# Optimization experiments

Measured on AMD Instinct MI355X. Metric: run time of the kernel, lower is better.

The kernel has to match this reference:

```python
import jax, jax.numpy as jnp
import numpy as np


def setup_inputs() -> dict:
    key = jax.random.key(0)
    kx, ky = jax.random.split(key)
    B, N, M = 32, 2048, 2048
    x = jax.random.normal(kx, (B, N, 3), dtype=jnp.float32)
    y = jax.random.normal(ky, (B, M, 3), dtype=jnp.float32)
    return {"x": x, "y": y}


def reference(x, y):
    # Faithful Chamfer distance matching the torch module.
    # Note: the original removes rows that sum exactly to 0; with random
    # float inputs no such rows exist, so that step is a no-op here.
    # d[b, i, j] = ||x[b, j] - y[b, i]||^2, shape [B, M, N]
    d = jnp.sum((x[:, None, :, :] - y[:, :, None, :]) ** 2, axis=-1)
    # min over y for each x point (dim 0 in the per-item [M, N] matrix)
    x_min = jnp.min(d, axis=1)  # [B, N]
    # min over x for each y point (dim 1)
    y_min = jnp.min(d, axis=2)  # [B, M]
    per_item = jnp.mean(x_min, axis=1) + jnp.mean(y_min, axis=1)  # [B]
    return jnp.mean(per_item)
```

## Files before the change

### kernel.cpp

```cpp
#include <hip/hip_runtime.h>


#define B_  32
#define N_  2048
#define PTS (B_ * N_)
#define ONEB 0x3F80u

typedef short  bf16x8 __attribute__((ext_vector_type(8)));
typedef float  f32x16 __attribute__((ext_vector_type(16)));

__device__ __forceinline__ unsigned short f2b(float f) {
    unsigned u = __float_as_uint(f);
    return (unsigned short)((u + 0x7FFFu + ((u >> 16) & 1u)) >> 16);
}
__device__ __forceinline__ float b2f(unsigned short h) {
    return __uint_as_float(((unsigned)h) << 16);
}
#define PK(a, b) (((unsigned)(a)) | (((unsigned)(b)) << 16))

__device__ __forceinline__ float min16(const f32x16 d) {
    const float a = fminf(fminf(d[0],  d[1]),  d[2]);
    const float b = fminf(fminf(d[3],  d[4]),  d[5]);
    const float c = fminf(fminf(d[6],  d[7]),  d[8]);
    const float e = fminf(fminf(d[9],  d[10]), d[11]);
    const float f = fminf(fminf(d[12], d[13]), d[14]);
    const float g = fminf(fminf(a, b), c);
    const float i = fminf(fminf(e, f), d[15]);
    return fminf(g, i);
}

__global__ __launch_bounds__(512, 4) void chamfer_mfma_kernel(
    const float* __restrict__ x, const float* __restrict__ y,
    float* __restrict__ partial)
{
    __shared__ unsigned sB[N_ * 8];
    __shared__ float pm[2][4][64];
    __shared__ float sred[4];

    const int bid  = blockIdx.x;
    const int dir  = bid >> 8;
    const int b    = (bid >> 3) & 31;
    const int qg   = bid & 7;
    const int tid  = threadIdx.x;
    const int lane = tid & 63;
    const int wv   = tid >> 6;
    const int qs2  = wv & 3;
    const int half = wv >> 2;
    const int h    = lane >> 5;
    const int ln31 = lane & 31;

    const float* q = dir ? y : x;
    const float* r = dir ? x : y;
    const float* rb = r + (size_t)b * N_ * 3;
    const float* qb = q + ((size_t)b * N_ + qg * 256 + qs2 * 64) * 3;

    for (int p = tid; p < N_; p += 512) {
        const float vx = rb[3 * p + 0], vy = rb[3 * p + 1], vz = rb[3 * p + 2];
        const unsigned short xh = f2b(vx), xl = f2b(vx - b2f(xh));
        const unsigned short yh = f2b(vy), yl = f2b(vy - b2f(yh));
        const unsigned short zh = f2b(vz), zl = f2b(vz - b2f(zh));
        const float nrm = fmaf(vx, vx, fmaf(vy, vy, vz * vz));
        const unsigned short nh = f2b(nrm), nl = f2b(nrm - b2f(nh));
        const unsigned base = ((unsigned)(p >> 5)) * 256u + ((unsigned)(p & 31)) * 4u;
        const uint4 lo = make_uint4(PK(xh, xl), PK(xh, xl), PK(yh, yl), PK(yh, yl));
        const uint4 hi = make_uint4(PK(zh, zl), PK(zh, zl), PK(nh, nl), PK(ONEB, ONEB));
        *(uint4*)(sB + base)        = lo;
        *(uint4*)(sB + base + 128)  = hi;
    }

    bf16x8 bq[2];
    #pragma unroll
    for (int s = 0; s < 2; ++s) {
        const float* qp = qb + (size_t)(s * 32 + ln31) * 3;
        const float vx = qp[0], vy = qp[1], vz = qp[2];
        const unsigned short xh = f2b(vx), xl = f2b(vx - b2f(xh));
        const unsigned short yh = f2b(vy), yl = f2b(vy - b2f(yh));
        const unsigned short zh = f2b(vz), zl = f2b(vz - b2f(zh));
        const float nrm = fmaf(vx, vx, fmaf(vy, vy, vz * vz));
        const unsigned short nh = f2b(nrm), nl = f2b(nrm - b2f(nh));
        const unsigned short mxh = f2b(-2.0f * b2f(xh)), mxl = f2b(-2.0f * b2f(xl));
        const unsigned short myh = f2b(-2.0f * b2f(yh)), myl = f2b(-2.0f * b2f(yl));
        const unsigned short mzh = f2b(-2.0f * b2f(zh)), mzl = f2b(-2.0f * b2f(zl));
        unsigned u[4];
        if (h == 0) {
            u[0] = PK(mxh, mxh); u[1] = PK(mxl, mxl);
            u[2] = PK(myh, myh); u[3] = PK(myl, myl);
        } else {
            u[0] = PK(mzh, mzh); u[1] = PK(mzl, mzl);
            u[2] = PK(ONEB, ONEB); u[3] = PK(nh, nl);
        }
        bq[s] = *(bf16x8*)u;
    }
    __syncthreads();

    const f32x16 zacc = {};
    float mac00 = 3.4e38f, mac01 = 3.4e38f;
    float mac10 = 3.4e38f, mac11 = 3.4e38f;
    const unsigned roff = (unsigned)h * 128u + (unsigned)ln31 * 4u;
    const unsigned* sBh = sB + half * 32 * 256;

    #pragma unroll 2
    for (int t = 0; t < 32; ++t) {
        const bf16x8 af = *(const bf16x8*)(sBh + t * 256 + roff);
        const f32x16 d0 = __builtin_amdgcn_mfma_f32_32x32x16_bf16(af, bq[0], zacc, 0, 0, 0);
        const f32x16 d1 = __builtin_amdgcn_mfma_f32_32x32x16_bf16(af, bq[1], zacc, 0, 0, 0);
        if (t & 1) { mac01 = fminf(mac01, min16(d0)); mac11 = fminf(mac11, min16(d1)); }
        else       { mac00 = fminf(mac00, min16(d0)); mac10 = fminf(mac10, min16(d1)); }
    }

    float m0 = fminf(mac00, mac01);
    float m1 = fminf(mac10, mac11);
    m0 = fminf(m0, __shfl_xor(m0, 32));
    m1 = fminf(m1, __shfl_xor(m1, 32));
    if (lane < 32) {
        pm[half][qs2][ln31]      = m0;
        pm[half][qs2][32 + ln31] = m1;
    }
    __syncthreads();

    if (tid < 256) {
        const float v = fminf(pm[0][tid >> 6][tid & 63],
                              pm[1][tid >> 6][tid & 63]);
        float s = v;
        s += __shfl_xor(s, 1);
        s += __shfl_xor(s, 2);
        s += __shfl_xor(s, 4);
        s += __shfl_xor(s, 8);
        s += __shfl_xor(s, 16);
        s += __shfl_xor(s, 32);
        if (lane == 0) sred[tid >> 6] = s;
    }
    __syncthreads();
    if (tid == 0) partial[bid] = (sred[0] + sred[1]) + (sred[2] + sred[3]);
}

__global__ __launch_bounds__(256) void chamfer_final_kernel(
    const float* __restrict__ partial, float* __restrict__ out)
{
    const int tid = threadIdx.x;
    float s = partial[tid] + partial[tid + 256];
    #pragma unroll
    for (int off = 32; off > 0; off >>= 1) s += __shfl_down(s, off);
    __shared__ float sr[4];
    if ((tid & 63) == 0) sr[tid >> 6] = s;
    __syncthreads();
    if (tid == 0)
        out[0] = ((sr[0] + sr[1]) + (sr[2] + sr[3])) * (1.0f / (float)PTS);
}

extern "C" void kernel_launch(void* const* d_in, const int* in_sizes, int n_in,
                              void* d_out, int out_size, void* d_ws, size_t ws_size,
                              hipStream_t stream)
{
    const float* x = (const float*)d_in[0];
    const float* y = (const float*)d_in[1];
    float* partial = (float*)d_ws;
    float* out     = (float*)d_out;

    chamfer_mfma_kernel<<<512, 512, 0, stream>>>(x, y, partial);
    chamfer_final_kernel<<<1, 256, 0, stream>>>(partial, out);
}
```

Baseline: 16.94 us.

## Fuse final reduction via atomicAdd, vectorize reference loads, fully unroll MFMA loop

Removes the second reduction kernel by having each block atomically add its scaled partial sum into the output, which is zeroed with a memset beforehand. The reference-point staging loop now loads four points per thread with three float4 reads instead of scalar strided loads. The MFMA inner loop is fully unrolled and the row offset is folded into the base pointer. The atomic accumulation makes the summation order nondeterministic, adds a memset launch, and the full unroll raises register pressure.

```diff
diff --git a/kernel.cpp b/kernel.cpp
--- a/kernel.cpp
+++ b/kernel.cpp
@@ -31,7 +31,7 @@
 
 __global__ __launch_bounds__(512, 4) void chamfer_mfma_kernel(
     const float* __restrict__ x, const float* __restrict__ y,
-    float* __restrict__ partial)
+    float* __restrict__ out)
 {
     __shared__ unsigned sB[N_ * 8];
     __shared__ float pm[2][4][64];
@@ -54,18 +54,28 @@
     const float* rb = r + (size_t)b * N_ * 3;
     const float* qb = q + ((size_t)b * N_ + qg * 256 + qs2 * 64) * 3;
 
-    for (int p = tid; p < N_; p += 512) {
-        const float vx = rb[3 * p + 0], vy = rb[3 * p + 1], vz = rb[3 * p + 2];
-        const unsigned short xh = f2b(vx), xl = f2b(vx - b2f(xh));
-        const unsigned short yh = f2b(vy), yl = f2b(vy - b2f(yh));
-        const unsigned short zh = f2b(vz), zl = f2b(vz - b2f(zh));
-        const float nrm = fmaf(vx, vx, fmaf(vy, vy, vz * vz));
-        const unsigned short nh = f2b(nrm), nl = f2b(nrm - b2f(nh));
-        const unsigned base = ((unsigned)(p >> 5)) * 256u + ((unsigned)(p & 31)) * 4u;
-        const uint4 lo = make_uint4(PK(xh, xl), PK(xh, xl), PK(yh, yl), PK(yh, yl));
-        const uint4 hi = make_uint4(PK(zh, zl), PK(zh, zl), PK(nh, nl), PK(ONEB, ONEB));
-        *(uint4*)(sB + base)        = lo;
-        *(uint4*)(sB + base + 128)  = hi;
+    {
+        const int p0 = tid * 4;
+        const float4* src = (const float4*)(rb + 3 * p0);
+        const float4 v0 = src[0], v1 = src[1], v2 = src[2];
+        const float px[4] = {v0.x, v0.w, v1.z, v2.y};
+        const float py[4] = {v0.y, v1.x, v1.w, v2.z};
+        const float pz[4] = {v0.z, v1.y, v2.x, v2.w};
+        #pragma unroll
+        for (int k = 0; k < 4; ++k) {
+            const int p = p0 + k;
+            const float vx = px[k], vy = py[k], vz = pz[k];
+            const unsigned short xh = f2b(vx), xl = f2b(vx - b2f(xh));
+            const unsigned short yh = f2b(vy), yl = f2b(vy - b2f(yh));
+            const unsigned short zh = f2b(vz), zl = f2b(vz - b2f(zh));
+            const float nrm = fmaf(vx, vx, fmaf(vy, vy, vz * vz));
+            const unsigned short nh = f2b(nrm), nl = f2b(nrm - b2f(nh));
+            const unsigned base = ((unsigned)(p >> 5)) * 256u + ((unsigned)(p & 31)) * 4u;
+            *(uint4*)(sB + base) =
+                make_uint4(PK(xh, xl), PK(xh, xl), PK(yh, yl), PK(yh, yl));
+            *(uint4*)(sB + base + 128) =
+                make_uint4(PK(zh, zl), PK(zh, zl), PK(nh, nl), PK(ONEB, ONEB));
+        }
     }
 
     bf16x8 bq[2];
@@ -96,12 +106,12 @@
     const f32x16 zacc = {};
     float mac00 = 3.4e38f, mac01 = 3.4e38f;
     float mac10 = 3.4e38f, mac11 = 3.4e38f;
-    const unsigned roff = (unsigned)h * 128u + (unsigned)ln31 * 4u;
-    const unsigned* sBh = sB + half * 32 * 256;
+    const unsigned* sBh = sB + half * 32 * 256 +
+                          (unsigned)h * 128u + (unsigned)ln31 * 4u;
 
-    #pragma unroll 2
+    #pragma unroll 32
     for (int t = 0; t < 32; ++t) {
-        const bf16x8 af = *(const bf16x8*)(sBh + t * 256 + roff);
+        const bf16x8 af = *(const bf16x8*)(sBh + t * 256);
         const f32x16 d0 = __builtin_amdgcn_mfma_f32_32x32x16_bf16(af, bq[0], zacc, 0, 0, 0);
         const f32x16 d1 = __builtin_amdgcn_mfma_f32_32x32x16_bf16(af, bq[1], zacc, 0, 0, 0);
         if (t & 1) { mac01 = fminf(mac01, min16(d0)); mac11 = fminf(mac11, min16(d1)); }
@@ -131,21 +141,11 @@
         if (lane == 0) sred[tid >> 6] = s;
     }
     __syncthreads();
-    if (tid == 0) partial[bid] = (sred[0] + sred[1]) + (sred[2] + sred[3]);
-}
 
-__global__ __launch_bounds__(256) void chamfer_final_kernel(
-    const float* __restrict__ partial, float* __restrict__ out)
-{
-    const int tid = threadIdx.x;
-    float s = partial[tid] + partial[tid + 256];
-    #pragma unroll
-    for (int off = 32; off > 0; off >>= 1) s += __shfl_down(s, off);
-    __shared__ float sr[4];
-    if ((tid & 63) == 0) sr[tid >> 6] = s;
-    __syncthreads();
-    if (tid == 0)
-        out[0] = ((sr[0] + sr[1]) + (sr[2] + sr[3])) * (1.0f / (float)PTS);
+    if (tid == 0) {
+        const float bs = (sred[0] + sred[1]) + (sred[2] + sred[3]);
+        atomicAdd(out, bs * (1.0f / (float)PTS));
+    }
 }
 
 extern "C" void kernel_launch(void* const* d_in, const int* in_sizes, int n_in,
@@ -154,9 +154,8 @@
 {
     const float* x = (const float*)d_in[0];
     const float* y = (const float*)d_in[1];
-    float* partial = (float*)d_ws;
     float* out     = (float*)d_out;
 
-    chamfer_mfma_kernel<<<512, 512, 0, stream>>>(x, y, partial);
-    chamfer_final_kernel<<<1, 256, 0, stream>>>(partial, out);
+    hipMemsetAsync(out, 0, sizeof(float), stream);
+    chamfer_mfma_kernel<<<512, 512, 0, stream>>>(x, y, out);
 }
```

Result: slower. 23.02 us (+35.9%).
